# Kernel tuning notes

Hardware: AMD Instinct MI355X
Metric: run time of the kernel (lower is better)

Reference implementation:

```python
import jax, jax.numpy as jnp
import numpy as np

A = 0.5  # mixing coefficient `a` from __init__
B, S, C = 16, 4096, 512


def setup_inputs() -> dict:
    key = jax.random.key(0)
    k1, k2 = jax.random.split(key)
    predicted = jax.random.normal(k1, (B, S, C), dtype=jnp.float32)
    target = jax.random.randint(k2, (B, S), 0, C, dtype=jnp.int64)
    return {"predicted": predicted, "target": target}


def reference(predicted, target):
    # predicted: [B, S, C] logits, target: [B, S] int class ids.
    b, s, c = predicted.shape
    am = jnp.argmax(predicted, axis=-1)              # [B, S] per-position top-1 class (topk(1)[1])
    lse = jax.nn.logsumexp(predicted, axis=-1)       # [B, S]

    # counts[i, j, v] = #positions s with target[i,s]==j and argmax==v
    bidx = jnp.arange(b)[:, None]
    counts = jnp.zeros((b, c, c), dtype=jnp.int32).at[bidx, target, am].add(1)
    n = counts.sum(axis=-1)                          # [B, C] occurrences of class j in target[i]
    # torch.mode returns the smallest of the most common values; argmax over class value
    # returns the first (smallest) index achieving the max count, matching that tie-break.
    m = jnp.argmax(counts, axis=-1)                  # [B, C] mode label per (i, j)

    # pred_m[i, j, s] = predicted[i, s, m[i, j]]
    pred_m = predicted[jnp.arange(b)[:, None, None],
                       jnp.arange(s)[None, None, :],
                       m[:, :, None]]                # [B, C, S]
    # per-position CE against constant label m: lse - logit[m]
    term = lse[:, None, :] - pred_m                  # [B, C, S]

    maskT = target[:, None, :] == jnp.arange(c)[None, :, None]  # [B, C, S]
    eq_sum = jnp.sum(jnp.where(maskT, term, 0.0), axis=-1)      # [B, C]
    ne_sum = term.sum(axis=-1) - eq_sum                          # [B, C]

    nf = n.astype(predicted.dtype)
    present = n > 0
    eq_loss = eq_sum / jnp.maximum(nf, 1.0)
    ne_mean = ne_sum / jnp.maximum(s - nf, 1.0)
    ne_loss = 1.0 / jnp.where(present & (ne_mean != 0), ne_mean, 1.0)
    val = eq_loss * (1.0 - A) + A * ne_loss          # [B, C]

    keep = present & (val != 0)                      # cipherLoss[cipherLoss != 0]
    total = jnp.where(keep, val, 0.0).sum()
    cnt = jnp.maximum(keep.sum(), 1).astype(predicted.dtype)
    return total / cnt
```

## Files before the change

### kernel.cpp

```cpp
#include <hip/hip_runtime.h>
#include <cstdint>
#include <cstddef>

#define PB 16
#define PS 4096
#define PC 512

__global__ __launch_bounds__(256) void k0_init(float* __restrict__ colsum,
                                               float* __restrict__ acc,
                                               int* __restrict__ done) {
    int i = blockIdx.x * 256 + threadIdx.x;
    if (i < PB * PC) colsum[i] = 0.0f;
    if (i == 0) { acc[0] = 0.0f; acc[1] = 0.0f; *done = 0; }
}

__global__ __launch_bounds__(256) void k1_rows(const float* __restrict__ pred,
                                               int* __restrict__ am,
                                               float* __restrict__ lse,
                                               float* __restrict__ colsum) {
    const int t = threadIdx.x, w = t >> 6, l = t & 63;
    const int rowBase = blockIdx.x * 16 + w * 4;
    const int b = rowBase >> 12;
    const float* base = pred + (size_t)rowBase * PC + 4 * l;

    float4 va[4], vb[4];
    #pragma unroll
    for (int r = 0; r < 4; ++r) {
        va[r] = *(const float4*)(base + r * PC);
        vb[r] = *(const float4*)(base + r * PC + 256);
    }

    float mv[4]; int mi[4];
    #pragma unroll
    for (int r = 0; r < 4; ++r) {
        float m = va[r].x; int i0 = 4 * l;
        if (va[r].y > m) { m = va[r].y; i0 = 4 * l + 1; }
        if (va[r].z > m) { m = va[r].z; i0 = 4 * l + 2; }
        if (va[r].w > m) { m = va[r].w; i0 = 4 * l + 3; }
        if (vb[r].x > m) { m = vb[r].x; i0 = 256 + 4 * l; }
        if (vb[r].y > m) { m = vb[r].y; i0 = 256 + 4 * l + 1; }
        if (vb[r].z > m) { m = vb[r].z; i0 = 256 + 4 * l + 2; }
        if (vb[r].w > m) { m = vb[r].w; i0 = 256 + 4 * l + 3; }
        mv[r] = m; mi[r] = i0;
    }

    #pragma unroll
    for (int off = 1; off < 64; off <<= 1) {
        #pragma unroll
        for (int r = 0; r < 4; ++r) {
            float ov = __shfl_xor(mv[r], off, 64);
            int   oi = __shfl_xor(mi[r], off, 64);
            if (ov > mv[r] || (ov == mv[r] && oi < mi[r])) { mv[r] = ov; mi[r] = oi; }
        }
    }

    float ss[4];
    #pragma unroll
    for (int r = 0; r < 4; ++r) {
        ss[r] = __expf(va[r].x - mv[r]) + __expf(va[r].y - mv[r])
              + __expf(va[r].z - mv[r]) + __expf(va[r].w - mv[r])
              + __expf(vb[r].x - mv[r]) + __expf(vb[r].y - mv[r])
              + __expf(vb[r].z - mv[r]) + __expf(vb[r].w - mv[r]);
    }
    #pragma unroll
    for (int off = 1; off < 64; off <<= 1) {
        #pragma unroll
        for (int r = 0; r < 4; ++r) ss[r] += __shfl_xor(ss[r], off, 64);
    }

    float l0 = mv[0] + __logf(ss[0]);
    float l1 = mv[1] + __logf(ss[1]);
    float l2 = mv[2] + __logf(ss[2]);
    float l3 = mv[3] + __logf(ss[3]);

    if (l == 0) {
        *(float4*)(lse + rowBase) = make_float4(l0, l1, l2, l3);
        *(int4*)(am + rowBase) = make_int4(mi[0], mi[1], mi[2], mi[3]);
    }

    float cs0 = va[0].x + va[1].x + va[2].x + va[3].x;
    float cs1 = va[0].y + va[1].y + va[2].y + va[3].y;
    float cs2 = va[0].z + va[1].z + va[2].z + va[3].z;
    float cs3 = va[0].w + va[1].w + va[2].w + va[3].w;
    float cs4 = vb[0].x + vb[1].x + vb[2].x + vb[3].x;
    float cs5 = vb[0].y + vb[1].y + vb[2].y + vb[3].y;
    float cs6 = vb[0].z + vb[1].z + vb[2].z + vb[3].z;
    float cs7 = vb[0].w + vb[1].w + vb[2].w + vb[3].w;

    __shared__ float lds[4][PC];
    lds[w][4 * l + 0] = cs0; lds[w][4 * l + 1] = cs1;
    lds[w][4 * l + 2] = cs2; lds[w][4 * l + 3] = cs3;
    lds[w][256 + 4 * l + 0] = cs4; lds[w][256 + 4 * l + 1] = cs5;
    lds[w][256 + 4 * l + 2] = cs6; lds[w][256 + 4 * l + 3] = cs7;
    __syncthreads();
    for (int c = t; c < PC; c += 256) {
        float s = lds[0][c] + lds[1][c] + lds[2][c] + lds[3][c];
        atomicAdd(&colsum[(b << 9) + c], s);
    }
}

__global__ __launch_bounds__(512) void k_tail(const float* __restrict__ pred,
                                              const int* __restrict__ target,
                                              const int* __restrict__ am,
                                              const float* __restrict__ lse,
                                              const float* __restrict__ colsum,
                                              float* __restrict__ acc,
                                              int* __restrict__ done,
                                              float* __restrict__ out) {
    __shared__ int   tgam[PS];
    __shared__ float ldsLse[PS];
    __shared__ int   sbucket[PS];
    __shared__ int   sc[PC];
    __shared__ int   cur[PC];
    __shared__ float red[8], redv[8], redk[8];

    const int b = blockIdx.x, t = threadIdx.x;
    cur[t] = 0;
    __syncthreads();

    float lacc = 0.0f;
    for (int i = t; i < PS; i += 512) {
        int gi = (b << 12) + i;
        int tg = target[gi];
        int a  = am[gi];
        float lv = lse[gi];
        tgam[i] = tg | (a << 16);
        ldsLse[i] = lv;
        lacc += lv;
        atomicAdd(&cur[tg], 1);
    }
    #pragma unroll
    for (int off = 1; off < 64; off <<= 1) lacc += __shfl_xor(lacc, off, 64);
    if ((t & 63) == 0) red[t >> 6] = lacc;
    __syncthreads();
    float Ls = red[0] + red[1] + red[2] + red[3] + red[4] + red[5] + red[6] + red[7];

    int x = cur[t];
    sc[t] = x;
    __syncthreads();
    for (int off = 1; off < PC; off <<= 1) {
        int v = (t >= off) ? sc[t - off] : 0;
        __syncthreads();
        sc[t] += v;
        __syncthreads();
    }
    int start = sc[t] - x;
    cur[t] = start;
    __syncthreads();
    for (int i = t; i < PS; i += 512) {
        int e = tgam[i];
        int tg = e & 0xFFFF, a = e >> 16;
        int pos = atomicAdd(&cur[tg], 1);
        sbucket[pos] = i | (a << 12);
    }
    __syncthreads();

    int k = x;
    float val = 0.0f; int keep = 0;
    if (k > 0) {
        int bc = 0, bvv = 0;
        for (int i = 0; i < k; ++i) {
            int v = sbucket[start + i] >> 12;
            int c = 0;
            for (int j = 0; j < k; ++j) c += ((sbucket[start + j] >> 12) == v) ? 1 : 0;
            if (c > bc || (c == bc && v < bvv)) { bc = c; bvv = v; }
        }
        int m = bvv;
        float lseSum = 0.0f, ep = 0.0f;
        for (int i = 0; i < k; ++i) {
            int s = sbucket[start + i] & (PS - 1);
            lseSum += ldsLse[s];
            ep += pred[(((size_t)(b << 12)) + s) * PC + m];
        }
        float eq_sum = lseSum - ep;
        float ne_sum = (Ls - colsum[(b << 9) + m]) - eq_sum;
        float nf = (float)k;
        float eq_loss = eq_sum / fmaxf(nf, 1.0f);
        float ne_mean = ne_sum / fmaxf((float)PS - nf, 1.0f);
        float ne_loss = 1.0f / ((ne_mean != 0.0f) ? ne_mean : 1.0f);
        val = 0.5f * eq_loss + 0.5f * ne_loss;
        keep = (val != 0.0f) ? 1 : 0;
    }

    float vs = keep ? val : 0.0f;
    float ks = (float)keep;
    #pragma unroll
    for (int off = 1; off < 64; off <<= 1) {
        vs += __shfl_xor(vs, off, 64);
        ks += __shfl_xor(ks, off, 64);
    }
    if ((t & 63) == 0) { redv[t >> 6] = vs; redk[t >> 6] = ks; }
    __syncthreads();
    if (t == 0) {
        float sv = 0.0f, sk = 0.0f;
        #pragma unroll
        for (int i = 0; i < 8; ++i) { sv += redv[i]; sk += redk[i]; }
        atomicAdd(&acc[0], sv);
        atomicAdd(&acc[1], sk);
        __threadfence();
        int d = atomicAdd(done, 1);
        if (d == PB - 1) {
            __threadfence();
            float a0 = atomicAdd(&acc[0], 0.0f);
            float a1 = atomicAdd(&acc[1], 0.0f);
            out[0] = a0 / fmaxf(a1, 1.0f);
        }
    }
}

extern "C" void kernel_launch(void* const* d_in, const int* in_sizes, int n_in,
                              void* d_out, int out_size, void* d_ws, size_t ws_size,
                              hipStream_t stream) {
    const float* pred = (const float*)d_in[0];
    const int* target = (const int*)d_in[1];
    float* out = (float*)d_out;

    char* w = (char*)d_ws;
    int*   am     = (int*)(w + 0);
    float* lse    = (float*)(w + 262144);
    float* colsum = (float*)(w + 524288);
    float* acc    = (float*)(w + 557056);
    int*   done   = (int*)(w + 557064);

    k0_init<<<32, 256, 0, stream>>>(colsum, acc, done);
    k1_rows<<<(PB * PS) / 16, 256, 0, stream>>>(pred, am, lse, colsum);
    k_tail<<<PB, 512, 0, stream>>>(pred, target, am, lse, colsum, acc, done, out);
}
```

Measured before the change: 220.6 us.

## Fuse row pass and per-batch tail into one kernel via last-block tickets

Merges the row-statistics kernel and the per-batch tail kernel into a single launch. The last block to finish each batch, found through an atomic ticket counter, performs that batch's histogram, bucketing, mode search and loss. Zeroing is moved to a memset, the prefix scan becomes a wavefront shuffle scan, and the tail reads lse from global memory instead of staging it in LDS. This removes a kernel launch boundary and lets tail work overlap with rows still in flight. The tail now runs with 256 threads instead of 512, so each thread handles two classes serially, and lse/am are stored with atomic exchanges.

```diff
diff --git a/kernel.cpp b/kernel.cpp
--- a/kernel.cpp
+++ b/kernel.cpp
@@ -6,21 +6,27 @@
 #define PS 4096
 #define PC 512
 
-__global__ __launch_bounds__(256) void k0_init(float* __restrict__ colsum,
-                                               float* __restrict__ acc,
-                                               int* __restrict__ done) {
-    int i = blockIdx.x * 256 + threadIdx.x;
-    if (i < PB * PC) colsum[i] = 0.0f;
-    if (i == 0) { acc[0] = 0.0f; acc[1] = 0.0f; *done = 0; }
-}
-
-__global__ __launch_bounds__(256) void k1_rows(const float* __restrict__ pred,
-                                               int* __restrict__ am,
-                                               float* __restrict__ lse,
-                                               float* __restrict__ colsum) {
+__global__ __launch_bounds__(256) void k_main(const float* __restrict__ pred,
+                                              const int* __restrict__ target,
+                                              int* __restrict__ am,
+                                              float* __restrict__ lse,
+                                              float* __restrict__ colsum,
+                                              float* __restrict__ acc,
+                                              int* __restrict__ done,
+                                              int* __restrict__ bticket,
+                                              float* __restrict__ out) {
+    __shared__ float colred[4][PC];
+    __shared__ int   cnt[PC];
+    __shared__ int   offsA[PC];
+    __shared__ int   cur[PC];
+    __shared__ int   sbucket[PS];
+    __shared__ float fred[4];
+    __shared__ int   ired[4];
+    __shared__ int   isLast;
+
     const int t = threadIdx.x, w = t >> 6, l = t & 63;
     const int rowBase = blockIdx.x * 16 + w * 4;
-    const int b = rowBase >> 12;
+    const int b = blockIdx.x >> 8;
     const float* base = pred + (size_t)rowBase * PC + 4 * l;
 
     float4 va[4], vb[4];
@@ -68,133 +74,116 @@
         for (int r = 0; r < 4; ++r) ss[r] += __shfl_xor(ss[r], off, 64);
     }
 
-    float l0 = mv[0] + __logf(ss[0]);
-    float l1 = mv[1] + __logf(ss[1]);
-    float l2 = mv[2] + __logf(ss[2]);
-    float l3 = mv[3] + __logf(ss[3]);
-
     if (l == 0) {
-        *(float4*)(lse + rowBase) = make_float4(l0, l1, l2, l3);
-        *(int4*)(am + rowBase) = make_int4(mi[0], mi[1], mi[2], mi[3]);
-    }
-
-    float cs0 = va[0].x + va[1].x + va[2].x + va[3].x;
-    float cs1 = va[0].y + va[1].y + va[2].y + va[3].y;
-    float cs2 = va[0].z + va[1].z + va[2].z + va[3].z;
-    float cs3 = va[0].w + va[1].w + va[2].w + va[3].w;
-    float cs4 = vb[0].x + vb[1].x + vb[2].x + vb[3].x;
-    float cs5 = vb[0].y + vb[1].y + vb[2].y + vb[3].y;
-    float cs6 = vb[0].z + vb[1].z + vb[2].z + vb[3].z;
-    float cs7 = vb[0].w + vb[1].w + vb[2].w + vb[3].w;
-
-    __shared__ float lds[4][PC];
-    lds[w][4 * l + 0] = cs0; lds[w][4 * l + 1] = cs1;
-    lds[w][4 * l + 2] = cs2; lds[w][4 * l + 3] = cs3;
-    lds[w][256 + 4 * l + 0] = cs4; lds[w][256 + 4 * l + 1] = cs5;
-    lds[w][256 + 4 * l + 2] = cs6; lds[w][256 + 4 * l + 3] = cs7;
+        #pragma unroll
+        for (int r = 0; r < 4; ++r) {
+            atomicExch(&lse[rowBase + r], mv[r] + __logf(ss[r]));
+            atomicExch(&am[rowBase + r], mi[r]);
+        }
+    }
+
+    colred[w][4 * l + 0] = va[0].x + va[1].x + va[2].x + va[3].x;
+    colred[w][4 * l + 1] = va[0].y + va[1].y + va[2].y + va[3].y;
+    colred[w][4 * l + 2] = va[0].z + va[1].z + va[2].z + va[3].z;
+    colred[w][4 * l + 3] = va[0].w + va[1].w + va[2].w + va[3].w;
+    colred[w][256 + 4 * l + 0] = vb[0].x + vb[1].x + vb[2].x + vb[3].x;
+    colred[w][256 + 4 * l + 1] = vb[0].y + vb[1].y + vb[2].y + vb[3].y;
+    colred[w][256 + 4 * l + 2] = vb[0].z + vb[1].z + vb[2].z + vb[3].z;
+    colred[w][256 + 4 * l + 3] = vb[0].w + vb[1].w + vb[2].w + vb[3].w;
     __syncthreads();
     for (int c = t; c < PC; c += 256) {
-        float s = lds[0][c] + lds[1][c] + lds[2][c] + lds[3][c];
+        float s = colred[0][c] + colred[1][c] + colred[2][c] + colred[3][c];
         atomicAdd(&colsum[(b << 9) + c], s);
     }
-}
-
-__global__ __launch_bounds__(512) void k_tail(const float* __restrict__ pred,
-                                              const int* __restrict__ target,
-                                              const int* __restrict__ am,
-                                              const float* __restrict__ lse,
-                                              const float* __restrict__ colsum,
-                                              float* __restrict__ acc,
-                                              int* __restrict__ done,
-                                              float* __restrict__ out) {
-    __shared__ int   tgam[PS];
-    __shared__ float ldsLse[PS];
-    __shared__ int   sbucket[PS];
-    __shared__ int   sc[PC];
-    __shared__ int   cur[PC];
-    __shared__ float red[8], redv[8], redk[8];
-
-    const int b = blockIdx.x, t = threadIdx.x;
-    cur[t] = 0;
+
+    __threadfence();
+    __syncthreads();
+    if (t == 0) isLast = (atomicAdd(&bticket[b], 1) == 255) ? 1 : 0;
+    __syncthreads();
+    if (!isLast) return;
+    __threadfence();
+
+    cnt[t] = 0; cnt[t + 256] = 0;
     __syncthreads();
 
     float lacc = 0.0f;
-    for (int i = t; i < PS; i += 512) {
+    for (int i = t; i < PS; i += 256) {
+        int gi = (b << 12) + i;
+        atomicAdd(&cnt[target[gi]], 1);
+        lacc += lse[gi];
+    }
+    #pragma unroll
+    for (int off = 1; off < 64; off <<= 1) lacc += __shfl_xor(lacc, off, 64);
+    if (l == 0) fred[w] = lacc;
+    __syncthreads();
+    float Ls = fred[0] + fred[1] + fred[2] + fred[3];
+
+    int c0 = cnt[2 * t], c1 = cnt[2 * t + 1];
+    int s2 = c0 + c1, incl = s2;
+    #pragma unroll
+    for (int off = 1; off < 64; off <<= 1) {
+        int v = __shfl_up(incl, off, 64);
+        if (l >= off) incl += v;
+    }
+    if (l == 63) ired[w] = incl;
+    __syncthreads();
+    int woff = 0;
+    for (int j = 0; j < w; ++j) woff += ired[j];
+    incl += woff;
+    int e1 = incl - c1, e0 = e1 - c0;
+    offsA[2 * t] = e0; offsA[2 * t + 1] = e1;
+    cur[2 * t] = e0;   cur[2 * t + 1] = e1;
+    __syncthreads();
+
+    for (int i = t; i < PS; i += 256) {
         int gi = (b << 12) + i;
         int tg = target[gi];
         int a  = am[gi];
-        float lv = lse[gi];
-        tgam[i] = tg | (a << 16);
-        ldsLse[i] = lv;
-        lacc += lv;
-        atomicAdd(&cur[tg], 1);
-    }
-    #pragma unroll
-    for (int off = 1; off < 64; off <<= 1) lacc += __shfl_xor(lacc, off, 64);
-    if ((t & 63) == 0) red[t >> 6] = lacc;
-    __syncthreads();
-    float Ls = red[0] + red[1] + red[2] + red[3] + red[4] + red[5] + red[6] + red[7];
-
-    int x = cur[t];
-    sc[t] = x;
-    __syncthreads();
-    for (int off = 1; off < PC; off <<= 1) {
-        int v = (t >= off) ? sc[t - off] : 0;
-        __syncthreads();
-        sc[t] += v;
-        __syncthreads();
-    }
-    int start = sc[t] - x;
-    cur[t] = start;
-    __syncthreads();
-    for (int i = t; i < PS; i += 512) {
-        int e = tgam[i];
-        int tg = e & 0xFFFF, a = e >> 16;
         int pos = atomicAdd(&cur[tg], 1);
         sbucket[pos] = i | (a << 12);
     }
     __syncthreads();
 
-    int k = x;
-    float val = 0.0f; int keep = 0;
-    if (k > 0) {
-        int bc = 0, bvv = 0;
-        for (int i = 0; i < k; ++i) {
-            int v = sbucket[start + i] >> 12;
-            int c = 0;
-            for (int j = 0; j < k; ++j) c += ((sbucket[start + j] >> 12) == v) ? 1 : 0;
-            if (c > bc || (c == bc && v < bvv)) { bc = c; bvv = v; }
-        }
-        int m = bvv;
-        float lseSum = 0.0f, ep = 0.0f;
-        for (int i = 0; i < k; ++i) {
-            int s = sbucket[start + i] & (PS - 1);
-            lseSum += ldsLse[s];
-            ep += pred[(((size_t)(b << 12)) + s) * PC + m];
-        }
-        float eq_sum = lseSum - ep;
-        float ne_sum = (Ls - colsum[(b << 9) + m]) - eq_sum;
-        float nf = (float)k;
-        float eq_loss = eq_sum / fmaxf(nf, 1.0f);
-        float ne_mean = ne_sum / fmaxf((float)PS - nf, 1.0f);
-        float ne_loss = 1.0f / ((ne_mean != 0.0f) ? ne_mean : 1.0f);
-        val = 0.5f * eq_loss + 0.5f * ne_loss;
-        keep = (val != 0.0f) ? 1 : 0;
-    }
-
-    float vs = keep ? val : 0.0f;
-    float ks = (float)keep;
-    #pragma unroll
-    for (int off = 1; off < 64; off <<= 1) {
-        vs += __shfl_xor(vs, off, 64);
-        ks += __shfl_xor(ks, off, 64);
-    }
-    if ((t & 63) == 0) { redv[t >> 6] = vs; redk[t >> 6] = ks; }
+    float vsA = 0.0f, ksA = 0.0f;
+    for (int c = t; c < PC; c += 256) {
+        int k = cnt[c];
+        if (k > 0) {
+            int start = offsA[c];
+            int bc = 0, bvv = 0;
+            for (int i = 0; i < k; ++i) {
+                int v = sbucket[start + i] >> 12;
+                int cc = 0;
+                for (int j = 0; j < k; ++j) cc += ((sbucket[start + j] >> 12) == v) ? 1 : 0;
+                if (cc > bc || (cc == bc && v < bvv)) { bc = cc; bvv = v; }
+            }
+            int m = bvv;
+            float lseSum = 0.0f, ep = 0.0f;
+            for (int i = 0; i < k; ++i) {
+                int s = sbucket[start + i] & (PS - 1);
+                lseSum += lse[(b << 12) + s];
+                ep += pred[(((size_t)(b << 12)) + s) * PC + m];
+            }
+            float eq_sum = lseSum - ep;
+            float ne_sum = (Ls - colsum[(b << 9) + m]) - eq_sum;
+            float nf = (float)k;
+            float eq_loss = eq_sum / fmaxf(nf, 1.0f);
+            float ne_mean = ne_sum / fmaxf((float)PS - nf, 1.0f);
+            float ne_loss = 1.0f / ((ne_mean != 0.0f) ? ne_mean : 1.0f);
+            float val = 0.5f * eq_loss + 0.5f * ne_loss;
+            if (val != 0.0f) { vsA += val; ksA += 1.0f; }
+        }
+    }
+    #pragma unroll
+    for (int off = 1; off < 64; off <<= 1) {
+        vsA += __shfl_xor(vsA, off, 64);
+        ksA += __shfl_xor(ksA, off, 64);
+    }
+    if (l == 0) { fred[w] = vsA; ired[w] = __float_as_int(ksA); }
     __syncthreads();
     if (t == 0) {
-        float sv = 0.0f, sk = 0.0f;
-        #pragma unroll
-        for (int i = 0; i < 8; ++i) { sv += redv[i]; sk += redk[i]; }
+        float sv = fred[0] + fred[1] + fred[2] + fred[3];
+        float sk = __int_as_float(ired[0]) + __int_as_float(ired[1])
+                 + __int_as_float(ired[2]) + __int_as_float(ired[3]);
         atomicAdd(&acc[0], sv);
         atomicAdd(&acc[1], sk);
         __threadfence();
@@ -216,13 +205,14 @@
     float* out = (float*)d_out;
 
     char* w = (char*)d_ws;
-    int*   am     = (int*)(w + 0);
-    float* lse    = (float*)(w + 262144);
-    float* colsum = (float*)(w + 524288);
-    float* acc    = (float*)(w + 557056);
-    int*   done   = (int*)(w + 557064);
-
-    k0_init<<<32, 256, 0, stream>>>(colsum, acc, done);
-    k1_rows<<<(PB * PS) / 16, 256, 0, stream>>>(pred, am, lse, colsum);
-    k_tail<<<PB, 512, 0, stream>>>(pred, target, am, lse, colsum, acc, done, out);
+    int*   am      = (int*)(w + 0);
+    float* lse     = (float*)(w + 262144);
+    float* colsum  = (float*)(w + 524288);
+    float* acc     = (float*)(w + 557056);
+    int*   done    = (int*)(w + 557064);
+    int*   bticket = (int*)(w + 557072);
+
+    hipMemsetAsync(w + 524288, 0, 557072 + PB * 4 - 524288, stream);
+    k_main<<<(PB * PS) / 16, 256, 0, stream>>>(pred, target, am, lse, colsum,
+                                               acc, done, bticket, out);
 }
```

Result: slower. 829.1 us (+275.8%).

## Use nontemporal loads, unroll tail gather by two, replace init kernel with memset

Applied to the files above, without the earlier changes.

The row kernel now reads the 128MB logits tensor with nontemporal vector loads so the streamed data does not pollute the cache. The tail kernel's gather of pred[s, m] is unrolled by two with split accumulators, giving more memory-level parallelism on the latency-bound strided loads. The zero-init kernel is replaced by a hipMemsetAsync over the colsum, acc and done region. The summation order of the gathered logits changes slightly, and a memset may or may not be cheaper than a tiny kernel launch.

```diff
diff --git a/kernel.cpp b/kernel.cpp
--- a/kernel.cpp
+++ b/kernel.cpp
@@ -6,13 +6,7 @@
 #define PS 4096
 #define PC 512
 
-__global__ __launch_bounds__(256) void k0_init(float* __restrict__ colsum,
-                                               float* __restrict__ acc,
-                                               int* __restrict__ done) {
-    int i = blockIdx.x * 256 + threadIdx.x;
-    if (i < PB * PC) colsum[i] = 0.0f;
-    if (i == 0) { acc[0] = 0.0f; acc[1] = 0.0f; *done = 0; }
-}
+typedef float vf4 __attribute__((ext_vector_type(4)));
 
 __global__ __launch_bounds__(256) void k1_rows(const float* __restrict__ pred,
                                                int* __restrict__ am,
@@ -23,11 +17,11 @@
     const int b = rowBase >> 12;
     const float* base = pred + (size_t)rowBase * PC + 4 * l;
 
-    float4 va[4], vb[4];
+    vf4 va[4], vb[4];
     #pragma unroll
     for (int r = 0; r < 4; ++r) {
-        va[r] = *(const float4*)(base + r * PC);
-        vb[r] = *(const float4*)(base + r * PC + 256);
+        va[r] = __builtin_nontemporal_load((const vf4*)(base + r * PC));
+        vb[r] = __builtin_nontemporal_load((const vf4*)(base + r * PC + 256));
     }
 
     float mv[4]; int mi[4];
@@ -166,13 +160,23 @@
             if (c > bc || (c == bc && v < bvv)) { bc = c; bvv = v; }
         }
         int m = bvv;
-        float lseSum = 0.0f, ep = 0.0f;
-        for (int i = 0; i < k; ++i) {
-            int s = sbucket[start + i] & (PS - 1);
-            lseSum += ldsLse[s];
-            ep += pred[(((size_t)(b << 12)) + s) * PC + m];
-        }
-        float eq_sum = lseSum - ep;
+        float lseSum = 0.0f;
+        float ep0 = 0.0f, ep1 = 0.0f;
+        const float* pb = pred + (size_t)(b << 12) * PC + m;
+        int i = 0;
+        for (; i + 1 < k; i += 2) {
+            int s0 = sbucket[start + i] & (PS - 1);
+            int s1 = sbucket[start + i + 1] & (PS - 1);
+            lseSum += ldsLse[s0] + ldsLse[s1];
+            ep0 += pb[(size_t)s0 * PC];
+            ep1 += pb[(size_t)s1 * PC];
+        }
+        if (i < k) {
+            int s0 = sbucket[start + i] & (PS - 1);
+            lseSum += ldsLse[s0];
+            ep0 += pb[(size_t)s0 * PC];
+        }
+        float eq_sum = lseSum - (ep0 + ep1);
         float ne_sum = (Ls - colsum[(b << 9) + m]) - eq_sum;
         float nf = (float)k;
         float eq_loss = eq_sum / fmaxf(nf, 1.0f);
@@ -194,7 +198,7 @@
     if (t == 0) {
         float sv = 0.0f, sk = 0.0f;
         #pragma unroll
-        for (int i = 0; i < 8; ++i) { sv += redv[i]; sk += redk[i]; }
+        for (int i2 = 0; i2 < 8; ++i2) { sv += redv[i2]; sk += redk[i2]; }
         atomicAdd(&acc[0], sv);
         atomicAdd(&acc[1], sk);
         __threadfence();
@@ -222,7 +226,7 @@
     float* acc    = (float*)(w + 557056);
     int*   done   = (int*)(w + 557064);
 
-    k0_init<<<32, 256, 0, stream>>>(colsum, acc, done);
+    (void)hipMemsetAsync(w + 524288, 0, 32768 + 12, stream);
     k1_rows<<<(PB * PS) / 16, 256, 0, stream>>>(pred, am, lse, colsum);
     k_tail<<<PB, 512, 0, stream>>>(pred, target, am, lse, colsum, acc, done, out);
 }
```

After: 223.1 us. No clear change (+1.1%).
